# Kernel tuning notes

Hardware: AMD Instinct MI355X
Metric: run time of the kernel (lower is better)

Reference implementation:

```python
import jax, jax.numpy as jnp
import numpy as np


def dct_matrices(N):
    # torch_dct-style unnormalized DCT-II (norm=None): X_k = 2 * sum_n x_n cos(pi*(2n+1)k/(2N))
    n = jnp.arange(N, dtype=jnp.float32)
    ang = jnp.pi * (2.0 * n[None, :] + 1.0) * n[:, None] / (2.0 * N)  # [k, n]
    D = 2.0 * jnp.cos(ang)                                            # forward DCT matrix [k, n]
    w = jnp.where(n == 0, 0.5, 1.0)                                   # half-weight on DC term
    M = (jnp.cos(ang).T * w[None, :]) / (2.0 * N)                     # inverse DCT matrix [n, k]
    return D, M


def setup_inputs() -> dict:
    key = jax.random.key(0)
    k1, k2, k3 = jax.random.split(key, 3)
    B, c_in, c_out, H, W, kh, kw = 8, 64, 128, 128, 128, 5, 5
    K = float(np.sqrt(1.0 / (c_in * kh * kw)))
    x = jax.random.normal(k1, (B, c_in, H, W), dtype=jnp.float32)
    weight = (2.0 * jax.random.uniform(k2, (c_out, c_in, kh, kw), dtype=jnp.float32) - 1.0) * K
    bias = (2.0 * jax.random.uniform(k3, (c_out,), dtype=jnp.float32) - 1.0) * K
    return {"x": x, "weight": weight, "bias": bias}


def reference(x, weight, bias):
    B, c_in, H, W = x.shape
    c_out, _, kh, kw = weight.shape
    D, M = dct_matrices(H)

    # DCT-II along H axis of input
    xd = jnp.einsum('kh,bchw->bckw', D, x)            # (B, c_in, H, W)
    xf = jnp.fft.rfft(xd, axis=-1)                    # (B, c_in, H, Wf) complex

    # Pad kernel along H to full size, DCT along H, rFFT along W with n=W
    wpad = jnp.pad(weight, ((0, 0), (0, 0), (0, H - kh), (0, 0)))
    wd = jnp.einsum('kh,oihw->oikw', D, wpad)         # (c_out, c_in, H, kw)
    wf = jnp.fft.rfft(wd, n=W, axis=-1)               # (c_out, c_in, H, Wf) complex

    # Broadcast complex multiply + reduce over c_in (fused via einsum)
    hf = jnp.einsum('bchw,ochw->bohw', xf, wf)        # (B, c_out, H, Wf)
    h = jnp.fft.irfft(hf, n=W, axis=-1)               # (B, c_out, H, W)

    # Inverse DCT along H, add bias, stride slice (stride = 1)
    h = jnp.einsum('nk,bokw->bonw', M, h) + bias[None, :, None, None]
    return h[:, :, ::1, ::1]
```

## Files before the change

kernel.cpp:

```cpp
#include <hip/hip_runtime.h>


using half8v = __attribute__((ext_vector_type(8))) _Float16;
using half4v = __attribute__((ext_vector_type(4))) _Float16;
using f32x4  = __attribute__((ext_vector_type(4))) float;

#define PI_F 3.14159265358979323846f

__device__ __forceinline__ int sw_off(int n, int k, int K, int mask) {
    int c = k >> 3;
    return n * K + (((c ^ (n & mask)) << 3) | (k & 7));
}

__device__ __forceinline__ void gload16(const _Float16* g, _Float16* l) {
    __builtin_amdgcn_global_load_lds((const __attribute__((address_space(1))) void*)g,
                                     (__attribute__((address_space(3))) void*)l, 16, 0, 0);
}

__global__ __launch_bounds__(256) void k_prep(const float* __restrict__ w,
                                              _Float16* __restrict__ WD,
                                              _Float16* __restrict__ D,
                                              _Float16* __restrict__ M) {
    __shared__ float lw[1600];
    __shared__ float lcos[320];
    int co = blockIdx.x >> 1, k0 = (blockIdx.x & 1) << 6;
    int tid = threadIdx.x;

    for (int e = tid; e < 1600; e += 256) lw[e] = w[co * 1600 + e];
    for (int e = tid; e < 320; e += 256) {
        int kl = e / 5, i = e - kl * 5;
        lcos[e] = 2.0f * cosf(PI_F * (float)((2 * i + 1) * (k0 + kl)) * (1.0f / 256.0f));
    }
    if (tid < 64) {
        int g = blockIdx.x * 64 + tid;
        int k = g >> 7, h = g & 127;
        float ang = PI_F * (float)((2 * h + 1) * k) * (1.0f / 256.0f);
        float c = cosf(ang);
        D[k * 128 + h] = (_Float16)(2.0f * c);
        float wk = (k == 0) ? 0.5f : 1.0f;
        M[h * 128 + k] = (_Float16)(c * wk * (1.0f / 256.0f));
    }
    __syncthreads();

    for (int e = tid; e < 20480; e += 256) {
        int kk = e & 31, rest = e >> 5;
        int s = rest % 10, kl = rest / 10;
        int j = s >> 1, ci = ((s & 1) << 5) + kk;
        const float* wp = &lw[ci * 25 + j];
        const float* cp = &lcos[kl * 5];
        float acc = 0.f;
#pragma unroll
        for (int i = 0; i < 5; ++i) acc += cp[i] * wp[i * 5];
        WD[(((long)(k0 + kl) * 10 + s) * 128 + co) * 32 + kk] = (_Float16)acc;
    }
}

__device__ __forceinline__ void gemm128_gA(const _Float16* __restrict__ gA,
                                           const _Float16* lB,
                                           f32x4 acc[4][4], int tid) {
    int lane = tid & 63, ln = lane & 15, q = lane >> 4;
    int wave = tid >> 6, wm = wave >> 1, wn = wave & 1;
#pragma unroll
    for (int s = 0; s < 4; ++s) {
        half8v af[4], bf[4];
#pragma unroll
        for (int mt = 0; mt < 4; ++mt) {
            int m = wm * 64 + mt * 16 + ln;
            af[mt] = *(const half8v*)(&gA[m * 128 + (s * 4 + q) * 8]);
        }
#pragma unroll
        for (int nt = 0; nt < 4; ++nt) {
            int n = wn * 64 + nt * 16 + ln;
            bf[nt] = *(const half8v*)(&lB[n * 128 + (((s * 4 + q) ^ (n & 15)) << 3)]);
        }
#pragma unroll
        for (int mt = 0; mt < 4; ++mt)
#pragma unroll
            for (int nt = 0; nt < 4; ++nt)
                acc[mt][nt] = __builtin_amdgcn_mfma_f32_16x16x32_f16(af[mt], bf[nt], acc[mt][nt], 0, 0, 0);
    }
}

__device__ __forceinline__ void stage_transB(const _Float16* __restrict__ src, int row_stride,
                                             _Float16* l, int K, int mask, int nblocks, int tid) {
    for (int blk = tid; blk < nblocks; blk += 256) {
        int kb = blk >> 4, wb = blk & 15;
        int k0 = kb * 4, w0 = wb * 8;
        half8v r0 = *(const half8v*)(&src[(k0 + 0) * row_stride + w0]);
        half8v r1 = *(const half8v*)(&src[(k0 + 1) * row_stride + w0]);
        half8v r2 = *(const half8v*)(&src[(k0 + 2) * row_stride + w0]);
        half8v r3 = *(const half8v*)(&src[(k0 + 3) * row_stride + w0]);
#pragma unroll
        for (int dw = 0; dw < 8; ++dw) {
            int n = w0 + dw;
            half4v p = {r0[dw], r1[dw], r2[dw], r3[dw]};
            *(half4v*)(&l[sw_off(n, k0, K, mask)]) = p;
        }
    }
}

__global__ __launch_bounds__(256) void k_dctH(const float* __restrict__ x,
                                              const _Float16* __restrict__ Dg,
                                              _Float16* __restrict__ xd) {
    __shared__ __align__(16) _Float16 lB[128 * 128];
    int b = blockIdx.x >> 6, ci = blockIdx.x & 63;
    int tid = threadIdx.x;

    const float* xs = x + (long)(b * 64 + ci) * 16384;
#pragma unroll
    for (int rep = 0; rep < 2; ++rep) {
        int blk = tid + rep * 256;
        int hb = blk >> 4, wb = blk & 15;
        int h0 = hb * 4, w0 = wb * 8;
        f32x4 f[4][2];
#pragma unroll
        for (int dh = 0; dh < 4; ++dh) {
            f[dh][0] = *(const f32x4*)(&xs[(h0 + dh) * 128 + w0]);
            f[dh][1] = *(const f32x4*)(&xs[(h0 + dh) * 128 + w0 + 4]);
        }
#pragma unroll
        for (int dw = 0; dw < 8; ++dw) {
            int n = w0 + dw;
            half4v p = {(_Float16)f[0][dw >> 2][dw & 3], (_Float16)f[1][dw >> 2][dw & 3],
                        (_Float16)f[2][dw >> 2][dw & 3], (_Float16)f[3][dw >> 2][dw & 3]};
            *(half4v*)(&lB[sw_off(n, h0, 128, 15)]) = p;
        }
    }
    __syncthreads();

    f32x4 acc[4][4] = {};
    gemm128_gA(Dg, lB, acc, tid);

    int lane = tid & 63, ln = lane & 15, q = lane >> 4;
    int wave = tid >> 6, wm = wave >> 1, wn = wave & 1;
#pragma unroll
    for (int mt = 0; mt < 4; ++mt)
#pragma unroll
        for (int nt = 0; nt < 4; ++nt)
#pragma unroll
            for (int r = 0; r < 4; ++r) {
                int kk = wm * 64 + mt * 16 + q * 4 + r;
                int wcol = wn * 64 + nt * 16 + ln;
                xd[((long)(kk * 8 + b) * 64 + ci) * 128 + wcol] = (_Float16)acc[mt][nt][r];
            }
}

__global__ __launch_bounds__(256) void k_conv(const _Float16* __restrict__ xd,
                                              const _Float16* __restrict__ WD,
                                              _Float16* __restrict__ y2) {
    __shared__ __align__(16) _Float16 lX[128 * 64];
    __shared__ __align__(16) _Float16 lW[3 * 4096];
    int bid = blockIdx.x;
    int k = bid & 127, b = bid >> 7;
    int tid = threadIdx.x;
    int lane = tid & 63, wave = tid >> 6;

    const _Float16* xs = xd + (long)(k * 8 + b) * 8192;
    stage_transB(xs, 128, lX, 64, 7, 256, tid);

    const _Float16* wkb = WD + (long)k * 40960;
    int eo = wave * 512 + lane * 8;
    gload16(&wkb[eo],        &lW[wave * 512]);
    gload16(&wkb[2048 + eo], &lW[2048 + wave * 512]);
    gload16(&wkb[4096 + eo], &lW[4096 + wave * 512]);
    gload16(&wkb[6144 + eo], &lW[4096 + 2048 + wave * 512]);
    __syncthreads();

    int ln = lane & 15, q = lane >> 4;
    int wm = wave >> 1, wn = wave & 1;
    f32x4 acc[4][4] = {};

    int rbuf = 0;
    for (int s = 0; s < 10; ++s) {
        if (s == 9) asm volatile("s_waitcnt vmcnt(0)" ::: "memory");
        else        asm volatile("s_waitcnt vmcnt(2)" ::: "memory");
        __builtin_amdgcn_s_barrier();
        asm volatile("" ::: "memory");

        const _Float16* wt = &lW[rbuf * 4096];
        int j = s >> 1;
        int cb = (s & 1) << 2;
        half8v af[4], bf[4];
#pragma unroll
        for (int mt = 0; mt < 4; ++mt) {
            int m = wm * 64 + mt * 16 + ln;
            af[mt] = *(const half8v*)(&wt[m * 32 + q * 8]);
        }
#pragma unroll
        for (int nt = 0; nt < 4; ++nt) {
            int wcol = wn * 64 + nt * 16 + ln;
            int n = (wcol - j) & 127;
            bf[nt] = *(const half8v*)(&lX[n * 64 + (((cb + q) ^ (n & 7)) << 3)]);
        }
        __builtin_amdgcn_s_setprio(1);
#pragma unroll
        for (int mt = 0; mt < 4; ++mt)
#pragma unroll
            for (int nt = 0; nt < 4; ++nt)
                acc[mt][nt] = __builtin_amdgcn_mfma_f32_16x16x32_f16(af[mt], bf[nt], acc[mt][nt], 0, 0, 0);
        __builtin_amdgcn_s_setprio(0);
        asm volatile("" ::: "memory");

        if (s < 8) {
            int wbuf = (rbuf == 0) ? 2 : rbuf - 1;
            const _Float16* gs = wkb + (s + 2) * 4096;
            gload16(&gs[eo],        &lW[wbuf * 4096 + wave * 512]);
            gload16(&gs[2048 + eo], &lW[wbuf * 4096 + 2048 + wave * 512]);
        }
        rbuf = (rbuf == 2) ? 0 : rbuf + 1;
    }

    _Float16* yb = y2 + (long)b * 2097152 + k * 128;
#pragma unroll
    for (int mt = 0; mt < 4; ++mt)
#pragma unroll
        for (int nt = 0; nt < 4; ++nt)
#pragma unroll
            for (int r = 0; r < 4; ++r) {
                int co = wm * 64 + mt * 16 + q * 4 + r;
                int wcol = wn * 64 + nt * 16 + ln;
                yb[(long)co * 16384 + wcol] = (_Float16)acc[mt][nt][r];
            }
}

__global__ __launch_bounds__(256, 4) void k_idct(const _Float16* __restrict__ y2,
                                                 const _Float16* __restrict__ Mg,
                                                 const float* __restrict__ bias,
                                                 float* __restrict__ out) {
    __shared__ __align__(16) _Float16 lB[128 * 128];
    int b = blockIdx.x >> 7, co = blockIdx.x & 127;
    int tid = threadIdx.x;

    const _Float16* src = y2 + (long)b * 2097152 + (long)co * 16384;
    stage_transB(src, 128, lB, 128, 15, 512, tid);
    __syncthreads();

    f32x4 acc[4][4] = {};
    gemm128_gA(Mg, lB, acc, tid);

    float bv = bias[co];
    float* ob = out + ((long)(b * 128 + co)) * 16384;
    int lane = tid & 63, ln = lane & 15, q = lane >> 4;
    int wave = tid >> 6, wm = wave >> 1, wn = wave & 1;
#pragma unroll
    for (int mt = 0; mt < 4; ++mt)
#pragma unroll
        for (int nt = 0; nt < 4; ++nt)
#pragma unroll
            for (int r = 0; r < 4; ++r) {
                int h = wm * 64 + mt * 16 + q * 4 + r;
                int wcol = wn * 64 + nt * 16 + ln;
                __builtin_nontemporal_store(acc[mt][nt][r] + bv, &ob[h * 128 + wcol]);
            }
}

extern "C" void kernel_launch(void* const* d_in, const int* in_sizes, int n_in,
                              void* d_out, int out_size, void* d_ws, size_t ws_size,
                              hipStream_t stream) {
    const float* x    = (const float*)d_in[0];
    const float* w    = (const float*)d_in[1];
    const float* bias = (const float*)d_in[2];
    float* out = (float*)d_out;

    char* ws = (char*)d_ws;
    _Float16* D  = (_Float16*)(ws);
    _Float16* M  = (_Float16*)(ws + 32768);
    _Float16* WD = (_Float16*)(ws + 65536);
    _Float16* xd = (_Float16*)(ws + 65536 + 10485760);
    _Float16* y2 = (_Float16*)(ws + 65536 + 10485760 + 16777216);

    k_prep<<<dim3(256),  dim3(256), 0, stream>>>(w, WD, D, M);
    k_dctH<<<dim3(512),  dim3(256), 0, stream>>>(x, D, xd);
    k_conv<<<dim3(1024), dim3(256), 0, stream>>>(xd, WD, y2);
    k_idct<<<dim3(1024), dim3(256), 0, stream>>>(y2, M, bias, out);
}
```

Baseline: 166.5 us.

## Switch to XOR-fold LDS swizzle, double-buffer conv weights, drop idct hints

Replaces the row-mask LDS swizzle with a folded 3-bit XOR swizzle shared by all staging and fragment reads. The conv kernel's weight ring shrinks from three to two LDS buffers, with a second barrier added before each refill. This cuts LDS per block, which may allow more resident blocks, at the cost of an extra barrier per step. The idct kernel also drops its min-blocks launch bound and uses ordinary stores instead of nontemporal ones.

```diff
diff --git a/kernel.cpp b/kernel.cpp
--- a/kernel.cpp
+++ b/kernel.cpp
@@ -7,9 +7,11 @@
 
 #define PI_F 3.14159265358979323846f
 
-__device__ __forceinline__ int sw_off(int n, int k, int K, int mask) {
+__device__ __forceinline__ int swz(int n) { return (n ^ (n >> 3)) & 7; }
+
+__device__ __forceinline__ int sw_off(int n, int k, int K) {
     int c = k >> 3;
-    return n * K + (((c ^ (n & mask)) << 3) | (k & 7));
+    return n * K + (((c ^ swz(n)) << 3) | (k & 7));
 }
 
 __device__ __forceinline__ void gload16(const _Float16* g, _Float16* l) {
@@ -71,7 +73,7 @@
 #pragma unroll
         for (int nt = 0; nt < 4; ++nt) {
             int n = wn * 64 + nt * 16 + ln;
-            bf[nt] = *(const half8v*)(&lB[n * 128 + (((s * 4 + q) ^ (n & 15)) << 3)]);
+            bf[nt] = *(const half8v*)(&lB[n * 128 + (((s * 4 + q) ^ swz(n)) << 3)]);
         }
 #pragma unroll
         for (int mt = 0; mt < 4; ++mt)
@@ -82,7 +84,7 @@
 }
 
 __device__ __forceinline__ void stage_transB(const _Float16* __restrict__ src, int row_stride,
-                                             _Float16* l, int K, int mask, int nblocks, int tid) {
+                                             _Float16* l, int K, int nblocks, int tid) {
     for (int blk = tid; blk < nblocks; blk += 256) {
         int kb = blk >> 4, wb = blk & 15;
         int k0 = kb * 4, w0 = wb * 8;
@@ -94,7 +96,7 @@
         for (int dw = 0; dw < 8; ++dw) {
             int n = w0 + dw;
             half4v p = {r0[dw], r1[dw], r2[dw], r3[dw]};
-            *(half4v*)(&l[sw_off(n, k0, K, mask)]) = p;
+            *(half4v*)(&l[sw_off(n, k0, K)]) = p;
         }
     }
 }
@@ -123,7 +125,7 @@
             int n = w0 + dw;
             half4v p = {(_Float16)f[0][dw >> 2][dw & 3], (_Float16)f[1][dw >> 2][dw & 3],
                         (_Float16)f[2][dw >> 2][dw & 3], (_Float16)f[3][dw >> 2][dw & 3]};
-            *(half4v*)(&lB[sw_off(n, h0, 128, 15)]) = p;
+            *(half4v*)(&lB[sw_off(n, h0, 128)]) = p;
         }
     }
     __syncthreads();
@@ -149,14 +151,14 @@
                                               const _Float16* __restrict__ WD,
                                               _Float16* __restrict__ y2) {
     __shared__ __align__(16) _Float16 lX[128 * 64];
-    __shared__ __align__(16) _Float16 lW[3 * 4096];
+    __shared__ __align__(16) _Float16 lW[2 * 4096];
     int bid = blockIdx.x;
     int k = bid & 127, b = bid >> 7;
     int tid = threadIdx.x;
     int lane = tid & 63, wave = tid >> 6;
 
     const _Float16* xs = xd + (long)(k * 8 + b) * 8192;
-    stage_transB(xs, 128, lX, 64, 7, 256, tid);
+    stage_transB(xs, 128, lX, 64, 256, tid);
 
     const _Float16* wkb = WD + (long)k * 40960;
     int eo = wave * 512 + lane * 8;
@@ -170,14 +172,13 @@
     int wm = wave >> 1, wn = wave & 1;
     f32x4 acc[4][4] = {};
 
-    int rbuf = 0;
     for (int s = 0; s < 10; ++s) {
         if (s == 9) asm volatile("s_waitcnt vmcnt(0)" ::: "memory");
         else        asm volatile("s_waitcnt vmcnt(2)" ::: "memory");
         __builtin_amdgcn_s_barrier();
         asm volatile("" ::: "memory");
 
-        const _Float16* wt = &lW[rbuf * 4096];
+        const _Float16* wt = &lW[(s & 1) * 4096];
         int j = s >> 1;
         int cb = (s & 1) << 2;
         half8v af[4], bf[4];
@@ -190,7 +191,7 @@
         for (int nt = 0; nt < 4; ++nt) {
             int wcol = wn * 64 + nt * 16 + ln;
             int n = (wcol - j) & 127;
-            bf[nt] = *(const half8v*)(&lX[n * 64 + (((cb + q) ^ (n & 7)) << 3)]);
+            bf[nt] = *(const half8v*)(&lX[n * 64 + (((cb + q) ^ swz(n)) << 3)]);
         }
         __builtin_amdgcn_s_setprio(1);
 #pragma unroll
@@ -199,15 +200,14 @@
             for (int nt = 0; nt < 4; ++nt)
                 acc[mt][nt] = __builtin_amdgcn_mfma_f32_16x16x32_f16(af[mt], bf[nt], acc[mt][nt], 0, 0, 0);
         __builtin_amdgcn_s_setprio(0);
+
         asm volatile("" ::: "memory");
-
+        __builtin_amdgcn_s_barrier();
         if (s < 8) {
-            int wbuf = (rbuf == 0) ? 2 : rbuf - 1;
             const _Float16* gs = wkb + (s + 2) * 4096;
-            gload16(&gs[eo],        &lW[wbuf * 4096 + wave * 512]);
-            gload16(&gs[2048 + eo], &lW[wbuf * 4096 + 2048 + wave * 512]);
-        }
-        rbuf = (rbuf == 2) ? 0 : rbuf + 1;
+            gload16(&gs[eo],        &lW[(s & 1) * 4096 + wave * 512]);
+            gload16(&gs[2048 + eo], &lW[(s & 1) * 4096 + 2048 + wave * 512]);
+        }
     }
 
     _Float16* yb = y2 + (long)b * 2097152 + k * 128;
@@ -223,16 +223,16 @@
             }
 }
 
-__global__ __launch_bounds__(256, 4) void k_idct(const _Float16* __restrict__ y2,
-                                                 const _Float16* __restrict__ Mg,
-                                                 const float* __restrict__ bias,
-                                                 float* __restrict__ out) {
+__global__ __launch_bounds__(256) void k_idct(const _Float16* __restrict__ y2,
+                                              const _Float16* __restrict__ Mg,
+                                              const float* __restrict__ bias,
+                                              float* __restrict__ out) {
     __shared__ __align__(16) _Float16 lB[128 * 128];
     int b = blockIdx.x >> 7, co = blockIdx.x & 127;
     int tid = threadIdx.x;
 
     const _Float16* src = y2 + (long)b * 2097152 + (long)co * 16384;
-    stage_transB(src, 128, lB, 128, 15, 512, tid);
+    stage_transB(src, 128, lB, 128, 512, tid);
     __syncthreads();
 
     f32x4 acc[4][4] = {};
@@ -250,7 +250,7 @@
             for (int r = 0; r < 4; ++r) {
                 int h = wm * 64 + mt * 16 + q * 4 + r;
                 int wcol = wn * 64 + nt * 16 + ln;
-                __builtin_nontemporal_store(acc[mt][nt][r] + bv, &ob[h * 128 + wcol]);
+                ob[h * 128 + wcol] = acc[mt][nt][r] + bv;
             }
 }
 
```

Result: faster. 146.5 us (-12.0%).
